# Optimization experiments

Measured on AMD Instinct MI355X. Metric: run time of the kernel, lower is better.

## Reference

```python
import jax, jax.numpy as jnp
import numpy as np
import math

PHI = (1 + math.sqrt(5)) / 2
B, T, D, H = 2, 2048, 1024, 16
DH = D // H
DC = 1024
DFF = int(D * PHI)  # 1657


def setup_inputs() -> dict:
    key = jax.random.key(0)
    ks = jax.random.split(key, 16)
    n = lambda i, shape, s=0.02: jax.random.normal(ks[i], shape, jnp.float32) * s
    tril = jnp.tril(jnp.ones((T, T), bool))
    mask = jnp.where(tril, 0.0, -1e9).astype(jnp.float32)[None, None]  # causal additive
    return dict(
        x=jax.random.normal(ks[0], (B, T, D), jnp.float32),
        center_from_above=jax.random.normal(ks[1], (B, DC), jnp.float32),
        mask=mask,
        gate_w=n(2, (D, 1), 0.5), gate_b=jnp.zeros((1,), jnp.float32),
        cb_w=n(3, (DC, 1), 0.5),
        nf_g=jnp.ones((D,), jnp.float32), nf_b=jnp.zeros((D,), jnp.float32),
        wq=n(4, (D, D)), wk=n(5, (D, D)), wv=n(6, (D, D)), wo=n(7, (D, D)),
        phase=jnp.linspace(0.0, math.pi, H).astype(jnp.float32),
        nb_g=jnp.ones((D,), jnp.float32), nb_b=jnp.zeros((D,), jnp.float32),
        up_w=n(8, (D, DFF)), up_b=jnp.zeros((DFF,), jnp.float32),
        dn_w=n(9, (DFF, D)), dn_b=jnp.zeros((D,), jnp.float32),
        commit_w=n(10, (D, 1)), commit_b=jnp.zeros((1,), jnp.float32),
        cproj_w=n(11, (D, DC)), cproj_b=jnp.zeros((DC,), jnp.float32),
        bcast_w=n(12, (DC, D)), bcast_b=jnp.zeros((D,), jnp.float32),
    )


def _ln(x, g, b, eps=1e-5):
    m = x.mean(-1, keepdims=True)
    v = ((x - m) ** 2).mean(-1, keepdims=True)
    return (x - m) * jax.lax.rsqrt(v + eps) * g + b


def _forward(x, center_from_above, mask, gate_w, gate_b, cb_w, nf_g, nf_b,
             wq, wk, wv, wo, phase, nb_g, nb_b, up_w, up_b, dn_w, dn_b,
             commit_w, commit_b, cproj_w, cproj_b, bcast_w, bcast_b):
    # broadcast center from above into the field
    x = x + (center_from_above @ bcast_w + bcast_b)[:, None, :]
    # binary aperture with straight-through estimator
    logits = x @ gate_w + gate_b + (center_from_above @ cb_w)[:, None, :]  # (B,T,1)
    prob = jax.nn.sigmoid(logits)
    hard = (prob > 0.5).astype(x.dtype)
    gate = hard - jax.lax.stop_gradient(prob) + prob
    h = _ln(x, nf_g, nf_b)
    heads = lambda w: (h @ w).reshape(B, T, H, DH).transpose(0, 2, 1, 3)  # (B,H,T,DH)
    Q, K, V = heads(wq), heads(wk), heads(wv)
    half = DH // 2
    c = jnp.cos(phase)[None, :, None, None]
    s = jnp.sin(phase)[None, :, None, None]
    def rot(z):
        re, im = z[..., :half], z[..., half:]
        return jnp.concatenate([re * c - im * s, re * s + im * c], axis=-1)
    Q, K = rot(Q), rot(K)
    ge = gate[:, None]  # (B,1,T,1)
    Q = Q * ge
    K = K * ge
    scores = jnp.einsum('bhqd,bhkd->bhqk', Q, K) / math.sqrt(DH) + mask
    attn = jax.nn.softmax(scores, axis=-1)
    fo = jnp.einsum('bhqk,bhkd->bhqd', attn, V).transpose(0, 2, 1, 3).reshape(B, T, D)
    fo = (fo @ wo) * gate
    x = x + fo
    h2 = _ln(x, nb_g, nb_b)
    ff = jax.nn.gelu(h2 @ up_w + up_b, approximate=False) @ dn_w + dn_b
    center_pool = x.mean(axis=1)  # (B,D)
    commit = jax.nn.sigmoid(center_pool @ commit_w + commit_b)  # (B,1)
    x = x + commit[:, None, :] * gate * ff
    center = jnp.tanh(center_pool @ cproj_w + cproj_b)  # (B,DC)
    return x, center, gate, commit


def reference(x, center_from_above, mask, gate_w, gate_b, cb_w, nf_g, nf_b,
              wq, wk, wv, wo, phase, nb_g, nb_b, up_w, up_b, dn_w, dn_b,
              commit_w, commit_b, cproj_w, cproj_b, bcast_w, bcast_b):
    return _forward(x, center_from_above, mask, gate_w, gate_b, cb_w, nf_g, nf_b,
                    wq, wk, wv, wo, phase, nb_g, nb_b, up_w, up_b, dn_w, dn_b,
                    commit_w, commit_b, cproj_w, cproj_b, bcast_w, bcast_b)
```

## Files before the change

kernel.cpp:

```cpp
#include <hip/hip_runtime.h>
#include <math.h>

#define B_   2
#define T_   2048
#define D_   1024
#define H_   16
#define DH_  64
#define DC_  1024
#define DFF_ 1656
#define DFFP_ 1664
#define MTOT 4096
#define NELEM_X 4194304ull

typedef short s16x8 __attribute__((ext_vector_type(8)));
typedef unsigned short u16x4 __attribute__((ext_vector_type(4)));
typedef float f32x4 __attribute__((ext_vector_type(4)));
typedef float f32x16 __attribute__((ext_vector_type(16)));
typedef unsigned short bfbits;

__device__ __forceinline__ bfbits f2bf(float f) {
  unsigned int u = __builtin_bit_cast(unsigned int, f);
  u += 0x7fffu + ((u >> 16) & 1u);
  return (bfbits)(u >> 16);
}

__device__ __forceinline__ float vexp2(float x) {
  float r;
  asm("v_exp_f32 %0, %1" : "=v"(r) : "v"(x));
  return r;
}
__device__ __forceinline__ unsigned pkbf(float lo, float hi) {
  unsigned r;
  asm("v_cvt_pk_bf16_f32 %0, %1, %2" : "=v"(r) : "v"(lo), "v"(hi));
  return r;
}

__device__ __forceinline__ void gload16(const void* g, void* l) {
  __builtin_amdgcn_global_load_lds(
      (__attribute__((address_space(1))) void*)g,
      (__attribute__((address_space(3))) void*)l, 16, 0, 0);
}

constexpr size_t OFF_X1   = 0;
constexpr size_t OFF_H    = OFF_X1 + 4ull*NELEM_X;
constexpr size_t OFF_Q    = OFF_H  + 2ull*NELEM_X;
constexpr size_t OFF_K    = OFF_Q  + 2ull*NELEM_X;
constexpr size_t OFF_VT   = OFF_K  + 2ull*NELEM_X;
constexpr size_t OFF_AO   = OFF_VT + 2ull*NELEM_X;
constexpr size_t OFF_X2   = OFF_AO + 2ull*NELEM_X;
constexpr size_t OFF_WQKV = OFF_X2 + 4ull*NELEM_X;
constexpr size_t OFF_WO   = OFF_WQKV + 3072ull*1024*2;
constexpr size_t OFF_WUP  = OFF_WO   + 1024ull*1024*2;
constexpr size_t OFF_WDN  = OFF_WUP  + 1664ull*1024*2;
constexpr size_t OFF_BVEC = OFF_WDN  + 1024ull*1664*2;
constexpr size_t OFF_CBV  = OFF_BVEC + 2048ull*4;
constexpr size_t OFF_GATE = OFF_CBV  + 256;
constexpr size_t OFF_PART = OFF_GATE + 4096ull*4;
constexpr size_t OFF_POOL = OFF_PART + 128ull*1024*4;
constexpr size_t OFF_CMT  = OFF_POOL + 2048ull*4;

__global__ __launch_bounds__(256)
void transpose_w(const float* __restrict__ src, bfbits* __restrict__ dst,
                 int R, int C, int Rpad, int Npad) {
  __shared__ float tile[32][33];
  const int kb = blockIdx.x * 32, nb = blockIdx.y * 32;
  const int tx = threadIdx.x & 31, ty = threadIdx.x >> 5;
  for (int i = ty; i < 32; i += 8) {
    const int k = kb + i, n = nb + tx;
    tile[i][tx] = (k < R && n < C) ? src[(size_t)k * C + n] : 0.f;
  }
  __syncthreads();
  for (int i = ty; i < 32; i += 8) {
    const int n = nb + i, k = kb + tx;
    if (n < Npad && k < Rpad) dst[(size_t)n * Rpad + k] = f2bf(tile[tx][i]);
  }
}

__global__ __launch_bounds__(256)
void gemv_t(const float* __restrict__ v, const float* __restrict__ w,
            const float* __restrict__ bias, float* __restrict__ out,
            int tanh_mode) {
  const int b = blockIdx.y;
  const int dl = threadIdx.x & 31, cl = threadIdx.x >> 5;
  const int d = blockIdx.x * 32 + dl;
  const float* vb = v + b * 1024;
  float s = 0.f;
  #pragma unroll 4
  for (int c = cl; c < 1024; c += 8)
    s += vb[c] * w[(size_t)c * 1024 + d];
  __shared__ float red[8][32];
  red[cl][dl] = s;
  __syncthreads();
  if (threadIdx.x < 32) {
    float t = 0.f;
    #pragma unroll
    for (int i = 0; i < 8; ++i) t += red[i][threadIdx.x];
    const int dd = blockIdx.x * 32 + threadIdx.x;
    t += bias[dd];
    out[b * 1024 + dd] = tanh_mode ? tanhf(t) : t;
  }
}

__global__ __launch_bounds__(256)
void cb_kernel(const float* __restrict__ cfa, const float* __restrict__ cbw,
               float* __restrict__ cbv) {
  const int b = blockIdx.x, tid = threadIdx.x;
  float4 a = *(const float4*)(cfa + b * 1024 + tid * 4);
  float4 w = *(const float4*)(cbw + tid * 4);
  float s = a.x * w.x + a.y * w.y + a.z * w.z + a.w * w.w;
  #pragma unroll
  for (int o = 32; o > 0; o >>= 1) s += __shfl_xor(s, o);
  __shared__ float ls[4];
  if ((tid & 63) == 0) ls[tid >> 6] = s;
  __syncthreads();
  if (tid == 0) cbv[b] = ls[0] + ls[1] + ls[2] + ls[3];
}

__device__ __forceinline__ void blockreduce3(float& a, float& b, float& c) {
  #pragma unroll
  for (int o = 32; o > 0; o >>= 1) {
    a += __shfl_xor(a, o);
    b += __shfl_xor(b, o);
    c += __shfl_xor(c, o);
  }
  __shared__ float ls[3][4];
  const int lane = threadIdx.x & 63, w = threadIdx.x >> 6;
  if (lane == 0) { ls[0][w] = a; ls[1][w] = b; ls[2][w] = c; }
  __syncthreads();
  a = ls[0][0] + ls[0][1] + ls[0][2] + ls[0][3];
  b = ls[1][0] + ls[1][1] + ls[1][2] + ls[1][3];
  c = ls[2][0] + ls[2][1] + ls[2][2] + ls[2][3];
}

__global__ __launch_bounds__(256)
void ln1_kernel(const float* __restrict__ x, const float* __restrict__ bvec,
                const float* __restrict__ cbv, const float* __restrict__ gw,
                const float* __restrict__ gb, const float* __restrict__ nfg,
                const float* __restrict__ nfb, float* __restrict__ x1,
                bfbits* __restrict__ h, float* __restrict__ gate_ws,
                float* __restrict__ gate_out) {
  const int m = blockIdx.x, tid = threadIdx.x, b = m >> 11;
  const size_t ro = (size_t)m * D_ + tid * 4;
  float4 xv = *(const float4*)(x + ro);
  float4 bv = *(const float4*)(bvec + b * D_ + tid * 4);
  float4 v;
  v.x = xv.x + bv.x; v.y = xv.y + bv.y; v.z = xv.z + bv.z; v.w = xv.w + bv.w;
  float4 g4 = *(const float4*)(gw + tid * 4);
  float s  = v.x + v.y + v.z + v.w;
  float s2 = v.x*v.x + v.y*v.y + v.z*v.z + v.w*v.w;
  float dg = v.x*g4.x + v.y*g4.y + v.z*g4.z + v.w*g4.w;
  blockreduce3(s, s2, dg);
  const float mean = s * (1.0f/1024.0f);
  const float var  = s2 * (1.0f/1024.0f) - mean*mean;
  const float rstd = rsqrtf(var + 1e-5f);
  if (tid == 0) {
    const float logits = dg + gb[0] + cbv[b];
    const float prob = 1.0f / (1.0f + expf(-logits));
    const float hard = prob > 0.5f ? 1.0f : 0.0f;
    const float gv = (hard - prob) + prob;
    gate_ws[m] = gv; gate_out[m] = gv;
  }
  *(float4*)(x1 + ro) = v;
  float4 gg = *(const float4*)(nfg + tid * 4);
  float4 b2 = *(const float4*)(nfb + tid * 4);
  u16x4 hv;
  hv[0] = f2bf((v.x - mean) * rstd * gg.x + b2.x);
  hv[1] = f2bf((v.y - mean) * rstd * gg.y + b2.y);
  hv[2] = f2bf((v.z - mean) * rstd * gg.z + b2.z);
  hv[3] = f2bf((v.w - mean) * rstd * gg.w + b2.w);
  *(u16x4*)(h + ro) = hv;
}

__global__ __launch_bounds__(256)
void ln2_kernel(const float* __restrict__ x2, const float* __restrict__ gptr,
                const float* __restrict__ bptr, bfbits* __restrict__ h2) {
  const int m = blockIdx.x, tid = threadIdx.x;
  const size_t ro = (size_t)m * D_ + tid * 4;
  float4 v = *(const float4*)(x2 + ro);
  float s  = v.x + v.y + v.z + v.w;
  float s2 = v.x*v.x + v.y*v.y + v.z*v.z + v.w*v.w;
  float d0 = 0.f;
  blockreduce3(s, s2, d0);
  const float mean = s * (1.0f/1024.0f);
  const float var  = s2 * (1.0f/1024.0f) - mean*mean;
  const float rstd = rsqrtf(var + 1e-5f);
  float4 gg = *(const float4*)(gptr + tid * 4);
  float4 b2 = *(const float4*)(bptr + tid * 4);
  u16x4 hv;
  hv[0] = f2bf((v.x - mean) * rstd * gg.x + b2.x);
  hv[1] = f2bf((v.y - mean) * rstd * gg.y + b2.y);
  hv[2] = f2bf((v.z - mean) * rstd * gg.z + b2.z);
  hv[3] = f2bf((v.w - mean) * rstd * gg.w + b2.w);
  *(u16x4*)(h2 + ro) = hv;
}

template <int EPI, int BM>
__global__ void __launch_bounds__(256, 2)
gemm_bt(const bfbits* __restrict__ A, int lda,
        const bfbits* __restrict__ Bt, int ldb, int K,
        const float* __restrict__ p0, const float* __restrict__ p1,
        const float* __restrict__ p2,
        float* __restrict__ fo0, const float* __restrict__ fo1,
        bfbits* __restrict__ bo0, bfbits* __restrict__ bo1,
        bfbits* __restrict__ bo2) {
  constexpr int MI = BM / 32;
  __shared__ bfbits Asl[2][BM * 32];
  __shared__ bfbits Bsl[2][128 * 32];
  const int tid = threadIdx.x;
  const int lane = tid & 63, wave = tid >> 6;
  const int g = lane >> 4, l15 = lane & 15;
  const int wr = wave >> 1, wc = wave & 1;
  const int m0 = blockIdx.y * BM, n0 = blockIdx.x * 128;

  auto stage = [&](int k0, int p) {
    #pragma unroll
    for (int i = 0; i < BM / 64; ++i) {
      const int c = i * 256 + tid;
      const int row = c >> 2;
      const int sw = (row & 3) ^ ((row >> 2) & 3);
      const int ko = ((c & 3) ^ sw) * 8;
      gload16(A + (size_t)(m0 + row) * lda + (k0 + ko),
              (char*)&Asl[p][0] + c * 16);
    }
    #pragma unroll
    for (int i = 0; i < 2; ++i) {
      const int c = i * 256 + tid;
      const int row = c >> 2;
      const int sw = (row & 3) ^ ((row >> 2) & 3);
      const int ko = ((c & 3) ^ sw) * 8;
      gload16(Bt + (size_t)(n0 + row) * ldb + (k0 + ko),
              (char*)&Bsl[p][0] + c * 16);
    }
  };

  f32x4 acc[MI][4] = {};
  stage(0, 0);
  __syncthreads();

  int t = 0;
  for (int k0 = 0; k0 < K; k0 += 32, ++t) {
    const int p = t & 1;
    if (k0 + 32 < K) stage(k0 + 32, p ^ 1);
    s16x8 af[MI], bfr[4];
    #pragma unroll
    for (int i = 0; i < MI; ++i) {
      const int row = wr * (MI * 16) + i * 16 + l15;
      const int sw = (row & 3) ^ ((row >> 2) & 3);
      af[i] = *(const s16x8*)&Asl[p][row * 32 + (g ^ sw) * 8];
    }
    #pragma unroll
    for (int i = 0; i < 4; ++i) {
      const int row = wc * 64 + i * 16 + l15;
      const int sw = (row & 3) ^ ((row >> 2) & 3);
      bfr[i] = *(const s16x8*)&Bsl[p][row * 32 + (g ^ sw) * 8];
    }
    #pragma unroll
    for (int i = 0; i < MI; ++i)
      #pragma unroll
      for (int j = 0; j < 4; ++j)
        acc[i][j] = __builtin_amdgcn_mfma_f32_16x16x32_bf16(af[i], bfr[j], acc[i][j], 0, 0, 0);
    __syncthreads();
  }

  const int b = m0 >> 11;
  const int trow0 = (m0 & 2047) + wr * (MI * 16);

  if constexpr (EPI == 0) {
    const float* gate = p0;
    const float* phase = p1;
    const int ncol0 = n0 + wc * 64;
    const int section = ncol0 >> 10;
    const int hh = (ncol0 & 1023) >> 6;
    if (section == 2) {
      bfbits* vt = bo2;
      const size_t vhead = (size_t)(b * H_ + hh) * DH_ * T_;
      #pragma unroll
      for (int mi = 0; mi < MI; ++mi) {
        const int tb = trow0 + mi * 16 + g * 4;
        #pragma unroll
        for (int ni = 0; ni < 4; ++ni) {
          const int dh = ni * 16 + l15;
          unsigned* dst32 = (unsigned*)&vt[vhead + (size_t)dh * T_ + tb];
          dst32[0] = pkbf(acc[mi][ni][0], acc[mi][ni][1]);
          dst32[1] = pkbf(acc[mi][ni][2], acc[mi][ni][3]);
        }
      }
    } else {
      const float cc = cosf(phase[hh]);
      const float ssn = sinf(phase[hh]);
      const float qs = (section == 0) ? 0.125f * 1.44269504088896341f : 1.0f;
      bfbits* dst = (section == 0) ? bo0 : bo1;
      const size_t head = (size_t)(b * H_ + hh) * T_ * DH_;
      #pragma unroll
      for (int mi = 0; mi < MI; ++mi) {
        const int tb = trow0 + mi * 16 + g * 4;
        float gv[4];
        #pragma unroll
        for (int r = 0; r < 4; ++r) gv[r] = gate[(size_t)b * T_ + tb + r] * qs;
        #pragma unroll
        for (int ni = 0; ni < 2; ++ni) {
          const int dh = ni * 16 + l15;
          #pragma unroll
          for (int r = 0; r < 4; ++r) {
            const float re = acc[mi][ni][r];
            const float im = acc[mi][ni + 2][r];
            const size_t idx = head + (size_t)(tb + r) * DH_ + dh;
            dst[idx]      = f2bf((re * cc - im * ssn) * gv[r]);
            dst[idx + 32] = f2bf((re * ssn + im * cc) * gv[r]);
          }
        }
      }
    }
  } else if constexpr (EPI == 1) {
    const float* gate = p0;
    const float* x1 = fo1;
    float* x2 = fo0;
    #pragma unroll
    for (int mi = 0; mi < MI; ++mi) {
      const int m = m0 + wr * (MI * 16) + mi * 16 + g * 4;
      float gv[4];
      #pragma unroll
      for (int r = 0; r < 4; ++r) gv[r] = gate[m + r];
      #pragma unroll
      for (int ni = 0; ni < 4; ++ni) {
        const int n = n0 + wc * 64 + ni * 16 + l15;
        #pragma unroll
        for (int r = 0; r < 4; ++r) {
          const size_t idx = (size_t)(m + r) * D_ + n;
          x2[idx] = x1[idx] + acc[mi][ni][r] * gv[r];
        }
      }
    }
  } else if constexpr (EPI == 2) {
    const float* upb = p0;
    bfbits* outm = bo0;
    #pragma unroll
    for (int mi = 0; mi < MI; ++mi) {
      const int m = m0 + wr * (MI * 16) + mi * 16 + g * 4;
      #pragma unroll
      for (int ni = 0; ni < 4; ++ni) {
        const int n = n0 + wc * 64 + ni * 16 + l15;
        const float bb = upb[n < DFF_ ? n : DFF_ - 1];
        #pragma unroll
        for (int r = 0; r < 4; ++r) {
          float v = acc[mi][ni][r] + bb;
          v = 0.5f * v * (1.0f + erff(v * 0.70710678118654752f));
          outm[(size_t)(m + r) * DFFP_ + n] = f2bf(v);
        }
      }
    }
  } else {
    const float* dnb = p0;
    const float* gate = p1;
    const float* cmt = p2;
    const float* x2 = fo1;
    float* outx = fo0;
    const float cb = cmt[b];
    #pragma unroll
    for (int mi = 0; mi < MI; ++mi) {
      const int m = m0 + wr * (MI * 16) + mi * 16 + g * 4;
      float kv[4];
      #pragma unroll
      for (int r = 0; r < 4; ++r) kv[r] = cb * gate[m + r];
      #pragma unroll
      for (int ni = 0; ni < 4; ++ni) {
        const int n = n0 + wc * 64 + ni * 16 + l15;
        const float bb = dnb[n];
        #pragma unroll
        for (int r = 0; r < 4; ++r) {
          const size_t idx = (size_t)(m + r) * D_ + n;
          outx[idx] = x2[idx] + kv[r] * (acc[mi][ni][r] + bb);
        }
      }
    }
  }
}

__global__ void __launch_bounds__(128, 2)
attn_kernel(const bfbits* __restrict__ Qb, const bfbits* __restrict__ Kb,
            const bfbits* __restrict__ Vt, bfbits* __restrict__ AO) {
  __shared__ bfbits Kl[2][64 * 64];
  __shared__ bfbits Vl[2][64 * 64];
  const int pid = blockIdx.x;
  const int bh = pid & 31;
  const int j = (pid >> 5) & 7;
  const int slot = pid >> 8;
  const int qt = (slot == 0) ? 31 - j
               : (slot == 1) ? 16 + j
               : (slot == 2) ? 15 - j : j;
  const int qb0 = qt * 64;
  const int tid = threadIdx.x, lane = tid & 63, wq = tid >> 6;
  const int l31 = lane & 31, hi = lane >> 5;
  const int qw = qb0 + wq * 32;

  const bfbits* Qp = Qb + ((size_t)bh * T_ + qw) * DH_;
  const bfbits* Kp = Kb + (size_t)bh * T_ * DH_;
  const bfbits* Vp = Vt + (size_t)bh * DH_ * T_;

  s16x8 qf[4];
  #pragma unroll
  for (int mf = 0; mf < 4; ++mf)
    qf[mf] = *(const s16x8*)(Qp + l31 * DH_ + mf * 16 + hi * 8);

  f32x16 o0 = {}, o1 = {};
  float mrun = -INFINITY, lrun = 0.f;
  const int nk = qt + 1;

  const bfbits* kg[4];
  const bfbits* vg[4];
  int cb_[4];
  #pragma unroll
  for (int i = 0; i < 4; ++i) {
    const int c = i * 128 + tid;
    const int row = c >> 3;
    const int sc = ((c & 7) ^ (row & 7)) * 8;
    kg[i] = Kp + row * DH_ + sc;
    vg[i] = Vp + (size_t)row * T_ + sc;
    cb_[i] = c * 16;
  }
  auto stage = [&](int k0, int p) {
    #pragma unroll
    for (int i = 0; i < 4; ++i) {
      gload16(kg[i] + (size_t)k0 * DH_, (char*)&Kl[p][0] + cb_[i]);
      gload16(vg[i] + k0,               (char*)&Vl[p][0] + cb_[i]);
    }
  };

  stage(0, 0);
  __syncthreads();

  for (int t = 0; t < nk; ++t) {
    const int p = t & 1;
    if (t + 1 < nk) stage((t + 1) << 6, p ^ 1);
    f32x16 s0 = {}, s1 = {};
    __builtin_amdgcn_s_setprio(1);
    #pragma unroll
    for (int mf = 0; mf < 4; ++mf) {
      const int ch = ((mf * 2 + hi) ^ (l31 & 7)) * 8;
      const s16x8 ka  = *(const s16x8*)&Kl[p][l31 * 64 + ch];
      const s16x8 kb2 = *(const s16x8*)&Kl[p][(32 + l31) * 64 + ch];
      s0 = __builtin_amdgcn_mfma_f32_32x32x16_bf16(ka,  qf[mf], s0, 0, 0, 0);
      s1 = __builtin_amdgcn_mfma_f32_32x32x16_bf16(kb2, qf[mf], s1, 0, 0, 0);
    }
    __builtin_amdgcn_s_setprio(0);
    if (t == nk - 1) {
      const int qd = wq * 32 + l31;
      #pragma unroll
      for (int r = 0; r < 16; ++r) {
        const int krow = (r & 3) + 8 * (r >> 2) + 4 * hi;
        if (krow > qd)      s0[r] = -1e9f;
        if (krow + 32 > qd) s1[r] = -1e9f;
      }
    }
    float red[8];
    #pragma unroll
    for (int i = 0; i < 8; ++i)
      red[i] = fmaxf(fmaxf(s0[i], s0[i + 8]), fmaxf(s1[i], s1[i + 8]));
    #pragma unroll
    for (int i = 0; i < 4; ++i) red[i] = fmaxf(red[i], red[i + 4]);
    float mx = fmaxf(fmaxf(red[0], red[1]), fmaxf(red[2], red[3]));
    mx = fmaxf(mx, __shfl_xor(mx, 32));
    const bool need = __any(mx > mrun + 8.f) != 0;
    const float mnew = need ? fmaxf(mrun, mx) : mrun;
    s0 = s0 - mnew;
    s1 = s1 - mnew;
    #pragma unroll
    for (int i = 0; i < 16; ++i) { s0[i] = vexp2(s0[i]); s1[i] = vexp2(s1[i]); }
    float sr[8];
    #pragma unroll
    for (int i = 0; i < 8; ++i)
      sr[i] = (s0[i] + s0[i + 8]) + (s1[i] + s1[i + 8]);
    #pragma unroll
    for (int i = 0; i < 4; ++i) sr[i] += sr[i + 4];
    float sum = (sr[0] + sr[1]) + (sr[2] + sr[3]);
    sum += __shfl_xor(sum, 32);
    if (need) {
      const float alpha = vexp2(mrun - mnew);
      mrun = mnew;
      lrun = lrun * alpha + sum;
      o0 *= alpha;
      o1 *= alpha;
    } else {
      lrun += sum;
    }
    #pragma unroll
    for (int mf = 0; mf < 4; ++mf) {
      const f32x16& s = (mf < 2) ? s0 : s1;
      const int r0 = (mf & 1) * 8;
      const unsigned A0 = pkbf(s[r0 + 0], s[r0 + 1]);
      const unsigned A1 = pkbf(s[r0 + 2], s[r0 + 3]);
      const unsigned B0 = pkbf(s[r0 + 4], s[r0 + 5]);
      const unsigned B1 = pkbf(s[r0 + 6], s[r0 + 7]);
      const unsigned x0 = (unsigned)__shfl_xor((int)(hi ? A0 : B0), 32);
      const unsigned x1 = (unsigned)__shfl_xor((int)(hi ? A1 : B1), 32);
      uint4 wv;
      wv.x = hi ? x0 : A0;
      wv.y = hi ? x1 : A1;
      wv.z = hi ? B0 : x0;
      wv.w = hi ? B1 : x1;
      const s16x8 pf = __builtin_bit_cast(s16x8, wv);
      const int ch = ((mf * 2 + hi) ^ (l31 & 7)) * 8;
      const s16x8 v0 = *(const s16x8*)&Vl[p][l31 * 64 + ch];
      const s16x8 v1 = *(const s16x8*)&Vl[p][(32 + l31) * 64 + ch];
      __builtin_amdgcn_s_setprio(1);
      o0 = __builtin_amdgcn_mfma_f32_32x32x16_bf16(v0, pf, o0, 0, 0, 0);
      o1 = __builtin_amdgcn_mfma_f32_32x32x16_bf16(v1, pf, o1, 0, 0, 0);
      __builtin_amdgcn_s_setprio(0);
    }
    __syncthreads();
  }

  const float inv = 1.0f / lrun;
  const int q = qw + l31;
  bfbits* dst = AO + ((size_t)(bh >> 4) * T_ + q) * D_ + (bh & 15) * DH_;
  #pragma unroll
  for (int rp = 0; rp < 8; ++rp) {
    const int dh = ((2 * rp) & 3) + 8 * (rp >> 1) + 4 * hi;
    *(unsigned*)(dst + dh)      = pkbf(o0[2 * rp] * inv, o0[2 * rp + 1] * inv);
    *(unsigned*)(dst + 32 + dh) = pkbf(o1[2 * rp] * inv, o1[2 * rp + 1] * inv);
  }
}

__global__ __launch_bounds__(256)
void pool_part(const float* __restrict__ x2, float* __restrict__ part) {
  const int s = blockIdx.x, b = blockIdx.y, tid = threadIdx.x;
  const float* base = x2 + ((size_t)b * T_ + s * 32) * D_ + tid * 4;
  float ax = 0, ay = 0, az = 0, aw = 0;
  #pragma unroll 4
  for (int t = 0; t < 32; ++t) {
    float4 v = *(const float4*)(base + (size_t)t * D_);
    ax += v.x; ay += v.y; az += v.z; aw += v.w;
  }
  float4 ov; ov.x = ax; ov.y = ay; ov.z = az; ov.w = aw;
  *(float4*)(part + (size_t)(b * 64 + s) * D_ + tid * 4) = ov;
}

__global__ __launch_bounds__(256)
void pool_fin(const float* __restrict__ part, float* __restrict__ pool) {
  const int idx = blockIdx.x * 256 + threadIdx.x;
  const int b = idx >> 10, d = idx & 1023;
  float s = 0.f;
  #pragma unroll 8
  for (int i = 0; i < 64; ++i) s += part[(size_t)(b * 64 + i) * D_ + d];
  pool[idx] = s * (1.0f / 2048.0f);
}

__global__ __launch_bounds__(256)
void commit_kernel(const float* __restrict__ pool, const float* __restrict__ cw,
                   const float* __restrict__ cb0, float* __restrict__ cmt,
                   float* __restrict__ out_cmt) {
  const int b = blockIdx.x, tid = threadIdx.x;
  float4 p = *(const float4*)(pool + b * 1024 + tid * 4);
  float4 w = *(const float4*)(cw + tid * 4);
  float s = p.x * w.x + p.y * w.y + p.z * w.z + p.w * w.w;
  #pragma unroll
  for (int o = 32; o > 0; o >>= 1) s += __shfl_xor(s, o);
  __shared__ float ls[4];
  if ((tid & 63) == 0) ls[tid >> 6] = s;
  __syncthreads();
  if (tid == 0) {
    const float t = ls[0] + ls[1] + ls[2] + ls[3] + cb0[0];
    const float v = 1.0f / (1.0f + expf(-t));
    cmt[b] = v; out_cmt[b] = v;
  }
}

extern "C" void kernel_launch(void* const* d_in, const int* in_sizes, int n_in,
                              void* d_out, int out_size, void* d_ws, size_t ws_size,
                              hipStream_t stream) {
  (void)in_sizes; (void)n_in; (void)out_size; (void)ws_size;
  const float* x       = (const float*)d_in[0];
  const float* cfa     = (const float*)d_in[1];
  const float* gate_w  = (const float*)d_in[3];
  const float* gate_b  = (const float*)d_in[4];
  const float* cb_w    = (const float*)d_in[5];
  const float* nf_g    = (const float*)d_in[6];
  const float* nf_b    = (const float*)d_in[7];
  const float* wq      = (const float*)d_in[8];
  const float* wk      = (const float*)d_in[9];
  const float* wv      = (const float*)d_in[10];
  const float* wo      = (const float*)d_in[11];
  const float* phase   = (const float*)d_in[12];
  const float* nb_g    = (const float*)d_in[13];
  const float* nb_b    = (const float*)d_in[14];
  const float* up_w    = (const float*)d_in[15];
  const float* up_b    = (const float*)d_in[16];
  const float* dn_w    = (const float*)d_in[17];
  const float* dn_b    = (const float*)d_in[18];
  const float* cmt_w   = (const float*)d_in[19];
  const float* cmt_b   = (const float*)d_in[20];
  const float* cproj_w = (const float*)d_in[21];
  const float* cproj_b = (const float*)d_in[22];
  const float* bcast_w = (const float*)d_in[23];
  const float* bcast_b = (const float*)d_in[24];

  char* ws = (char*)d_ws;
  float*  x1     = (float*)(ws + OFF_X1);
  bfbits* h      = (bfbits*)(ws + OFF_H);
  bfbits* h2     = (bfbits*)(ws + OFF_H);
  bfbits* qb     = (bfbits*)(ws + OFF_Q);
  bfbits* kb     = (bfbits*)(ws + OFF_K);
  bfbits* vt     = (bfbits*)(ws + OFF_VT);
  bfbits* ffmid  = (bfbits*)(ws + OFF_Q);
  bfbits* ao     = (bfbits*)(ws + OFF_AO);
  float*  x2     = (float*)(ws + OFF_X2);
  bfbits* wqkv_t = (bfbits*)(ws + OFF_WQKV);
  bfbits* wo_t   = (bfbits*)(ws + OFF_WO);
  bfbits* wup_t  = (bfbits*)(ws + OFF_WUP);
  bfbits* wdn_t  = (bfbits*)(ws + OFF_WDN);
  float*  bvec   = (float*)(ws + OFF_BVEC);
  float*  cbv    = (float*)(ws + OFF_CBV);
  float*  gate   = (float*)(ws + OFF_GATE);
  float*  part   = (float*)(ws + OFF_PART);
  float*  pool   = (float*)(ws + OFF_POOL);
  float*  cmt    = (float*)(ws + OFF_CMT);

  float* outx   = (float*)d_out;
  float* outc   = outx + NELEM_X;
  float* outg   = outc + B_ * DC_;
  float* outcmt = outg + B_ * T_;

  transpose_w<<<dim3(32, 32), 256, 0, stream>>>(wq, wqkv_t,                1024, 1024, 1024, 1024);
  transpose_w<<<dim3(32, 32), 256, 0, stream>>>(wk, wqkv_t + 1024 * 1024,  1024, 1024, 1024, 1024);
  transpose_w<<<dim3(32, 32), 256, 0, stream>>>(wv, wqkv_t + 2048 * 1024,  1024, 1024, 1024, 1024);
  transpose_w<<<dim3(32, 32), 256, 0, stream>>>(wo, wo_t,                  1024, 1024, 1024, 1024);
  transpose_w<<<dim3(32, 52), 256, 0, stream>>>(up_w, wup_t,               1024, DFF_, 1024, DFFP_);
  transpose_w<<<dim3(52, 32), 256, 0, stream>>>(dn_w, wdn_t,               DFF_, 1024, DFFP_, 1024);

  gemv_t<<<dim3(32, B_), 256, 0, stream>>>(cfa, bcast_w, bcast_b, bvec, 0);
  cb_kernel<<<B_, 256, 0, stream>>>(cfa, cb_w, cbv);

  ln1_kernel<<<MTOT, 256, 0, stream>>>(x, bvec, cbv, gate_w, gate_b, nf_g, nf_b,
                                       x1, h, gate, outg);

  gemm_bt<0, 128><<<dim3(24, 32), 256, 0, stream>>>(
      h, 1024, wqkv_t, 1024, 1024, gate, phase, nullptr,
      nullptr, nullptr, qb, kb, vt);

  attn_kernel<<<1024, 128, 0, stream>>>(qb, kb, vt, ao);

  gemm_bt<1, 64><<<dim3(8, 64), 256, 0, stream>>>(
      ao, 1024, wo_t, 1024, 1024, gate, nullptr, nullptr,
      x2, x1, nullptr, nullptr, nullptr);

  ln2_kernel<<<MTOT, 256, 0, stream>>>(x2, nb_g, nb_b, h2);

  pool_part<<<dim3(64, B_), 256, 0, stream>>>(x2, part);
  pool_fin<<<8, 256, 0, stream>>>(part, pool);
  commit_kernel<<<B_, 256, 0, stream>>>(pool, cmt_w, cmt_b, cmt, outcmt);
  gemv_t<<<dim3(32, B_), 256, 0, stream>>>(pool, cproj_w, cproj_b, outc, 1);

  gemm_bt<2, 64><<<dim3(13, 64), 256, 0, stream>>>(
      h2, 1024, wup_t, 1024, 1024, up_b, nullptr, nullptr,
      nullptr, nullptr, ffmid, nullptr, nullptr);

  gemm_bt<3, 64><<<dim3(8, 64), 256, 0, stream>>>(
      ffmid, DFFP_, wdn_t, DFFP_, DFFP_, dn_b, gate, cmt,
      outx, x2, nullptr, nullptr, nullptr);
}
```

Baseline: 258.3 us.

## Split long causal attention tiles across two blocks with merge; widen GEMM K-tile

Query tiles 16-31 of causal attention are split into two KV-range halves, scheduled through a constant job table across 1536 blocks, and recombined by a new merge kernel using saved row max/sum and unnormalized partial outputs. This is meant to balance per-block work and improve occupancy; the attention kernel also drops double-buffered K/V staging to a single buffer and raises the occupancy hint. GEMM kernels gain a BK template parameter, and the output, up and down projections use a 64-wide K step with a simpler XOR swizzle. The trade-offs are extra fp32 traffic for the partials, an extra launch, and loss of load/compute overlap in attention.

```diff
diff --git a/kernel.cpp b/kernel.cpp
--- a/kernel.cpp
+++ b/kernel.cpp
@@ -58,6 +58,19 @@
 constexpr size_t OFF_PART = OFF_GATE + 4096ull*4;
 constexpr size_t OFF_POOL = OFF_PART + 128ull*1024*4;
 constexpr size_t OFF_CMT  = OFF_POOL + 2048ull*4;
+constexpr size_t OFF_PM   = OFF_CMT  + 256;
+constexpr size_t OFF_PL   = OFF_PM   + 1024ull*64*4;
+
+__constant__ unsigned short JOBS[8][6] = {
+  {0x00F, 0x11C, 0x11A, 0x118, 0x006, 0x000},
+  {0x11E, 0x11D, 0x11B, 0x119, 0x005, 0x001},
+  {0x11F, 0x21D, 0x21B, 0x219, 0x004, 0x002},
+  {0x21F, 0x21C, 0x00B, 0x114, 0x008, 0x003},
+  {0x21E, 0x00C, 0x116, 0x009, 0x007, 0x210},
+  {0x00E, 0x117, 0x217, 0x110, 0x111, 0x211},
+  {0x00D, 0x218, 0x115, 0x112, 0x213, 0x212},
+  {0x21A, 0x215, 0x216, 0x00A, 0x113, 0x214},
+};
 
 __global__ __launch_bounds__(256)
 void transpose_w(const float* __restrict__ src, bfbits* __restrict__ dst,
@@ -194,7 +207,7 @@
   *(u16x4*)(h2 + ro) = hv;
 }
 
-template <int EPI, int BM>
+template <int EPI, int BM, int BK>
 __global__ void __launch_bounds__(256, 2)
 gemm_bt(const bfbits* __restrict__ A, int lda,
         const bfbits* __restrict__ Bt, int ldb, int K,
@@ -204,8 +217,10 @@
         bfbits* __restrict__ bo0, bfbits* __restrict__ bo1,
         bfbits* __restrict__ bo2) {
   constexpr int MI = BM / 32;
-  __shared__ bfbits Asl[2][BM * 32];
-  __shared__ bfbits Bsl[2][128 * 32];
+  constexpr int RCH = BK / 8;
+  constexpr int NK = BK / 32;
+  __shared__ bfbits Asl[2][BM * BK];
+  __shared__ bfbits Bsl[2][128 * BK];
   const int tid = threadIdx.x;
   const int lane = tid & 63, wave = tid >> 6;
   const int g = lane >> 4, l15 = lane & 15;
@@ -214,20 +229,18 @@
 
   auto stage = [&](int k0, int p) {
     #pragma unroll
-    for (int i = 0; i < BM / 64; ++i) {
+    for (int i = 0; i < (BM * RCH) / 256; ++i) {
       const int c = i * 256 + tid;
-      const int row = c >> 2;
-      const int sw = (row & 3) ^ ((row >> 2) & 3);
-      const int ko = ((c & 3) ^ sw) * 8;
+      const int row = c / RCH;
+      const int ko = ((c % RCH) ^ (row & (RCH - 1))) * 8;
       gload16(A + (size_t)(m0 + row) * lda + (k0 + ko),
               (char*)&Asl[p][0] + c * 16);
     }
     #pragma unroll
-    for (int i = 0; i < 2; ++i) {
+    for (int i = 0; i < (128 * RCH) / 256; ++i) {
       const int c = i * 256 + tid;
-      const int row = c >> 2;
-      const int sw = (row & 3) ^ ((row >> 2) & 3);
-      const int ko = ((c & 3) ^ sw) * 8;
+      const int row = c / RCH;
+      const int ko = ((c % RCH) ^ (row & (RCH - 1))) * 8;
       gload16(Bt + (size_t)(n0 + row) * ldb + (k0 + ko),
               (char*)&Bsl[p][0] + c * 16);
     }
@@ -238,27 +251,30 @@
   __syncthreads();
 
   int t = 0;
-  for (int k0 = 0; k0 < K; k0 += 32, ++t) {
+  for (int k0 = 0; k0 < K; k0 += BK, ++t) {
     const int p = t & 1;
-    if (k0 + 32 < K) stage(k0 + 32, p ^ 1);
-    s16x8 af[MI], bfr[4];
-    #pragma unroll
-    for (int i = 0; i < MI; ++i) {
-      const int row = wr * (MI * 16) + i * 16 + l15;
-      const int sw = (row & 3) ^ ((row >> 2) & 3);
-      af[i] = *(const s16x8*)&Asl[p][row * 32 + (g ^ sw) * 8];
-    }
-    #pragma unroll
-    for (int i = 0; i < 4; ++i) {
-      const int row = wc * 64 + i * 16 + l15;
-      const int sw = (row & 3) ^ ((row >> 2) & 3);
-      bfr[i] = *(const s16x8*)&Bsl[p][row * 32 + (g ^ sw) * 8];
-    }
-    #pragma unroll
-    for (int i = 0; i < MI; ++i)
-      #pragma unroll
-      for (int j = 0; j < 4; ++j)
-        acc[i][j] = __builtin_amdgcn_mfma_f32_16x16x32_bf16(af[i], bfr[j], acc[i][j], 0, 0, 0);
+    if (k0 + BK < K) stage(k0 + BK, p ^ 1);
+    s16x8 af[NK][MI], bfr[NK][4];
+    #pragma unroll
+    for (int kk = 0; kk < NK; ++kk) {
+      #pragma unroll
+      for (int i = 0; i < MI; ++i) {
+        const int row = wr * (MI * 16) + i * 16 + l15;
+        af[kk][i] = *(const s16x8*)&Asl[p][row * BK + (((kk * 4 + g) ^ (row & (RCH - 1))) * 8)];
+      }
+      #pragma unroll
+      for (int i = 0; i < 4; ++i) {
+        const int row = wc * 64 + i * 16 + l15;
+        bfr[kk][i] = *(const s16x8*)&Bsl[p][row * BK + (((kk * 4 + g) ^ (row & (RCH - 1))) * 8)];
+      }
+    }
+    #pragma unroll
+    for (int kk = 0; kk < NK; ++kk)
+      #pragma unroll
+      for (int i = 0; i < MI; ++i)
+        #pragma unroll
+        for (int j = 0; j < 4; ++j)
+          acc[i][j] = __builtin_amdgcn_mfma_f32_16x16x32_bf16(af[kk][i], bfr[kk][j], acc[i][j], 0, 0, 0);
     __syncthreads();
   }
 
@@ -376,18 +392,24 @@
   }
 }
 
-__global__ void __launch_bounds__(128, 2)
+__global__ void __launch_bounds__(128, 3)
 attn_kernel(const bfbits* __restrict__ Qb, const bfbits* __restrict__ Kb,
-            const bfbits* __restrict__ Vt, bfbits* __restrict__ AO) {
-  __shared__ bfbits Kl[2][64 * 64];
-  __shared__ bfbits Vl[2][64 * 64];
+            const bfbits* __restrict__ Vt, bfbits* __restrict__ AO,
+            float* __restrict__ pm, float* __restrict__ pl,
+            float* __restrict__ pO) {
+  __shared__ bfbits Kl[64 * 64];
+  __shared__ bfbits Vl[64 * 64];
   const int pid = blockIdx.x;
   const int bh = pid & 31;
   const int j = (pid >> 5) & 7;
   const int slot = pid >> 8;
-  const int qt = (slot == 0) ? 31 - j
-               : (slot == 1) ? 16 + j
-               : (slot == 2) ? 15 - j : j;
+  const unsigned job = JOBS[j][slot];
+  const int qt = job & 0xFF;
+  const int kind = job >> 8;
+  const int nk = qt + 1;
+  const int mid = (nk + 1) >> 1;
+  const int t0 = (kind == 2) ? mid : 0;
+  const int t1 = (kind == 1) ? mid : nk;
   const int qb0 = qt * 64;
   const int tid = threadIdx.x, lane = tid & 63, wq = tid >> 6;
   const int l31 = lane & 31, hi = lane >> 5;
@@ -404,7 +426,6 @@
 
   f32x16 o0 = {}, o1 = {};
   float mrun = -INFINITY, lrun = 0.f;
-  const int nk = qt + 1;
 
   const bfbits* kg[4];
   const bfbits* vg[4];
@@ -418,32 +439,27 @@
     vg[i] = Vp + (size_t)row * T_ + sc;
     cb_[i] = c * 16;
   }
-  auto stage = [&](int k0, int p) {
+
+  for (int t = t0; t < t1; ++t) {
+    const int k0 = t << 6;
     #pragma unroll
     for (int i = 0; i < 4; ++i) {
-      gload16(kg[i] + (size_t)k0 * DH_, (char*)&Kl[p][0] + cb_[i]);
-      gload16(vg[i] + k0,               (char*)&Vl[p][0] + cb_[i]);
-    }
-  };
-
-  stage(0, 0);
-  __syncthreads();
-
-  for (int t = 0; t < nk; ++t) {
-    const int p = t & 1;
-    if (t + 1 < nk) stage((t + 1) << 6, p ^ 1);
+      gload16(kg[i] + (size_t)k0 * DH_, (char*)&Kl[0] + cb_[i]);
+      gload16(vg[i] + k0,               (char*)&Vl[0] + cb_[i]);
+    }
+    __syncthreads();
     f32x16 s0 = {}, s1 = {};
     __builtin_amdgcn_s_setprio(1);
     #pragma unroll
     for (int mf = 0; mf < 4; ++mf) {
       const int ch = ((mf * 2 + hi) ^ (l31 & 7)) * 8;
-      const s16x8 ka  = *(const s16x8*)&Kl[p][l31 * 64 + ch];
-      const s16x8 kb2 = *(const s16x8*)&Kl[p][(32 + l31) * 64 + ch];
+      const s16x8 ka  = *(const s16x8*)&Kl[l31 * 64 + ch];
+      const s16x8 kb2 = *(const s16x8*)&Kl[(32 + l31) * 64 + ch];
       s0 = __builtin_amdgcn_mfma_f32_32x32x16_bf16(ka,  qf[mf], s0, 0, 0, 0);
       s1 = __builtin_amdgcn_mfma_f32_32x32x16_bf16(kb2, qf[mf], s1, 0, 0, 0);
     }
     __builtin_amdgcn_s_setprio(0);
-    if (t == nk - 1) {
+    if (t == qt) {
       const int qd = wq * 32 + l31;
       #pragma unroll
       for (int r = 0; r < 16; ++r) {
@@ -500,8 +516,8 @@
       wv.w = hi ? B1 : x1;
       const s16x8 pf = __builtin_bit_cast(s16x8, wv);
       const int ch = ((mf * 2 + hi) ^ (l31 & 7)) * 8;
-      const s16x8 v0 = *(const s16x8*)&Vl[p][l31 * 64 + ch];
-      const s16x8 v1 = *(const s16x8*)&Vl[p][(32 + l31) * 64 + ch];
+      const s16x8 v0 = *(const s16x8*)&Vl[l31 * 64 + ch];
+      const s16x8 v1 = *(const s16x8*)&Vl[(32 + l31) * 64 + ch];
       __builtin_amdgcn_s_setprio(1);
       o0 = __builtin_amdgcn_mfma_f32_32x32x16_bf16(v0, pf, o0, 0, 0, 0);
       o1 = __builtin_amdgcn_mfma_f32_32x32x16_bf16(v1, pf, o1, 0, 0, 0);
@@ -510,15 +526,53 @@
     __syncthreads();
   }
 
-  const float inv = 1.0f / lrun;
-  const int q = qw + l31;
-  bfbits* dst = AO + ((size_t)(bh >> 4) * T_ + q) * D_ + (bh & 15) * DH_;
-  #pragma unroll
-  for (int rp = 0; rp < 8; ++rp) {
-    const int dh = ((2 * rp) & 3) + 8 * (rp >> 1) + 4 * hi;
-    *(unsigned*)(dst + dh)      = pkbf(o0[2 * rp] * inv, o0[2 * rp + 1] * inv);
-    *(unsigned*)(dst + 32 + dh) = pkbf(o1[2 * rp] * inv, o1[2 * rp + 1] * inv);
-  }
+  if (kind == 0) {
+    const float inv = 1.0f / lrun;
+    const int q = qw + l31;
+    bfbits* dst = AO + ((size_t)(bh >> 4) * T_ + q) * D_ + (bh & 15) * DH_;
+    #pragma unroll
+    for (int rp = 0; rp < 8; ++rp) {
+      const int dh = ((2 * rp) & 3) + 8 * (rp >> 1) + 4 * hi;
+      *(unsigned*)(dst + dh)      = pkbf(o0[2 * rp] * inv, o0[2 * rp + 1] * inv);
+      *(unsigned*)(dst + 32 + dh) = pkbf(o1[2 * rp] * inv, o1[2 * rp + 1] * inv);
+    }
+  } else {
+    const int jid = ((qt - 16) * 32 + bh) * 2 + (kind - 1);
+    const int qloc = wq * 32 + l31;
+    pm[jid * 64 + qloc] = mrun;
+    pl[jid * 64 + qloc] = lrun;
+    float* po = pO + (size_t)jid * 4096;
+    #pragma unroll
+    for (int r = 0; r < 16; ++r) {
+      const int dh = (r & 3) + 8 * (r >> 2) + 4 * hi;
+      po[dh * 64 + qloc]        = o0[r];
+      po[(dh + 32) * 64 + qloc] = o1[r];
+    }
+  }
+}
+
+__global__ void __launch_bounds__(64)
+attn_merge(const float* __restrict__ pm, const float* __restrict__ pl,
+           const float* __restrict__ pO, bfbits* __restrict__ AO) {
+  __shared__ float lds[64][65];
+  const int u = blockIdx.x;
+  const int qt = 16 + (u >> 5), bh = u & 31;
+  const int q = threadIdx.x;
+  const int jA = ((qt - 16) * 32 + bh) * 2, jB = jA + 1;
+  const float mA = pm[jA * 64 + q], mB = pm[jB * 64 + q];
+  const float lA = pl[jA * 64 + q], lB = pl[jB * 64 + q];
+  const float m = fmaxf(mA, mB);
+  const float eA = vexp2(mA - m), eB = vexp2(mB - m);
+  const float inv = 1.0f / (lA * eA + lB * eB);
+  const float* OA = pO + (size_t)jA * 4096;
+  const float* OB = pO + (size_t)jB * 4096;
+  for (int dh = 0; dh < 64; ++dh)
+    lds[dh][q] = (OA[dh * 64 + q] * eA + OB[dh * 64 + q] * eB) * inv;
+  __syncthreads();
+  const int b = bh >> 4, hh = bh & 15;
+  bfbits* dst = AO + ((size_t)b * T_ + qt * 64) * D_ + hh * DH_ + q;
+  for (int qq = 0; qq < 64; ++qq)
+    dst[(size_t)qq * D_] = f2bf(lds[q][qq]);
 }
 
 __global__ __launch_bounds__(256)
@@ -604,6 +658,7 @@
   bfbits* ffmid  = (bfbits*)(ws + OFF_Q);
   bfbits* ao     = (bfbits*)(ws + OFF_AO);
   float*  x2     = (float*)(ws + OFF_X2);
+  float*  pO     = (float*)(ws + OFF_X2);
   bfbits* wqkv_t = (bfbits*)(ws + OFF_WQKV);
   bfbits* wo_t   = (bfbits*)(ws + OFF_WO);
   bfbits* wup_t  = (bfbits*)(ws + OFF_WUP);
@@ -614,6 +669,8 @@
   float*  part   = (float*)(ws + OFF_PART);
   float*  pool   = (float*)(ws + OFF_POOL);
   float*  cmt    = (float*)(ws + OFF_CMT);
+  float*  pm     = (float*)(ws + OFF_PM);
+  float*  pl     = (float*)(ws + OFF_PL);
 
   float* outx   = (float*)d_out;
   float* outc   = outx + NELEM_X;
@@ -633,13 +690,14 @@
   ln1_kernel<<<MTOT, 256, 0, stream>>>(x, bvec, cbv, gate_w, gate_b, nf_g, nf_b,
                                        x1, h, gate, outg);
 
-  gemm_bt<0, 128><<<dim3(24, 32), 256, 0, stream>>>(
+  gemm_bt<0, 128, 32><<<dim3(24, 32), 256, 0, stream>>>(
       h, 1024, wqkv_t, 1024, 1024, gate, phase, nullptr,
       nullptr, nullptr, qb, kb, vt);
 
-  attn_kernel<<<1024, 128, 0, stream>>>(qb, kb, vt, ao);
-
-  gemm_bt<1, 64><<<dim3(8, 64), 256, 0, stream>>>(
+  attn_kernel<<<1536, 128, 0, stream>>>(qb, kb, vt, ao, pm, pl, pO);
+  attn_merge<<<512, 64, 0, stream>>>(pm, pl, pO, ao);
+
+  gemm_bt<1, 64, 64><<<dim3(8, 64), 256, 0, stream>>>(
       ao, 1024, wo_t, 1024, 1024, gate, nullptr, nullptr,
       x2, x1, nullptr, nullptr, nullptr);
 
@@ -650,11 +708,11 @@
   commit_kernel<<<B_, 256, 0, stream>>>(pool, cmt_w, cmt_b, cmt, outcmt);
   gemv_t<<<dim3(32, B_), 256, 0, stream>>>(pool, cproj_w, cproj_b, outc, 1);
 
-  gemm_bt<2, 64><<<dim3(13, 64), 256, 0, stream>>>(
+  gemm_bt<2, 64, 64><<<dim3(13, 64), 256, 0, stream>>>(
       h2, 1024, wup_t, 1024, 1024, up_b, nullptr, nullptr,
       nullptr, nullptr, ffmid, nullptr, nullptr);
 
-  gemm_bt<3, 64><<<dim3(8, 64), 256, 0, stream>>>(
+  gemm_bt<3, 64, 64><<<dim3(8, 64), 256, 0, stream>>>(
       ffmid, DFFP_, wdn_t, DFFP_, DFFP_, dn_b, gate, cmt,
       outx, x2, nullptr, nullptr, nullptr);
 }
```

New measurement: 238.6 us. 1.08x faster.
